# Kernel optimization log

Hardware: AMD Instinct MI355X
Metric: run time of the kernel (lower is better)

## Reference

```python
import jax, jax.numpy as jnp
import numpy as np

B, IN, OUT = 32768, 64, 32
G, P = 8, 3              # bspline grid_size, order
TAY = 4                  # taylor_order
JDEG, JA, JB = 4, 1.0, 1.0
CDEG = 4
FREQ = 8
WCH = 4
TEMP = 2.0               # mix_temperature


def bspline_bases(x):
    # x: (B, In) -> (B, In, G+P)   Cox-de Boor with data-dependent uniform knots
    xmin = x.min(axis=0)
    xmax = x.max(axis=0)
    pad = (xmax - xmin) < 1e-8
    xmin = jnp.where(pad, xmin - 0.5, xmin)
    xmax = jnp.where(pad, xmax + 0.5, xmax)
    t = jnp.linspace(0.0, 1.0, G + 1, dtype=x.dtype)           # (G+1,)
    internal = xmin[:, None] + (xmax - xmin)[:, None] * t[None, :]  # (In, G+1)
    grid = jnp.concatenate([jnp.repeat(internal[:, :1], P, axis=1),
                            internal,
                            jnp.repeat(internal[:, -1:], P, axis=1)], axis=1)  # (In, G+2P+1)
    xe = x[:, :, None]
    bases = ((xe >= grid[:, :-1]) & (xe < grid[:, 1:])).astype(x.dtype)
    mask_last = x == grid[:, -1][None, :]                       # (B, In)
    bases = jnp.where(mask_last[:, :, None], 0.0, bases)
    bases = bases.at[..., -1].set(jnp.where(mask_last, 1.0, bases[..., -1]))
    for r in range(1, P + 1):
        ld = jnp.maximum(grid[:, r:-1] - grid[:, :-(r + 1)], 1e-12)
        rd = jnp.maximum(grid[:, r + 1:] - grid[:, 1:-r], 1e-12)
        left = (xe - grid[:, :-(r + 1)]) / ld * bases[..., :-1]
        right = (grid[:, r + 1:] - xe) / rd * bases[..., 1:]
        bases = left + right
    return bases


def taylor_bases(x):
    k = jnp.arange(TAY, dtype=x.dtype)
    fac = jnp.exp(jax.lax.lgamma(k + 1.0))
    return x[:, :, None] ** k / fac                             # (B, In, TAY)


def jacobi_bases(x):
    a, b = JA, JB
    terms = [jnp.ones_like(x)]
    if JDEG >= 1:
        terms.append(0.5 * (2.0 * (a + 1.0) * x + (a - b)) / np.sqrt(2.0))
    for n in range(2, JDEG + 1):
        k = n - 1
        A1 = 2 * k + a + b
        A2 = 2 * (k + 1) * (k + a + b + 1) * (A1 + 1)
        A3 = (A1 + 1) * ((A1 + 2) * A1 * x + a * a - b * b)
        A4 = 2 * (k + a) * (k + b) * (A1 + 2)
        Jn = A3 / A2 * terms[n - 1] - A4 / A2 * terms[n - 2]
        terms.append(Jn / np.sqrt(n + 1.0))
    return jnp.stack(terms, axis=-1)                            # (B, In, JDEG+1)


def cheby_bases(x):
    # project=True: sanitize + clamp
    xc = jnp.where(jnp.isfinite(x), x, 0.0)
    xc = jnp.clip(xc, -1e6, 1e6)
    terms = [jnp.ones_like(xc), xc]
    for _ in range(1, CDEG):
        terms.append(2.0 * xc * terms[-1] - terms[-2])
    T = jnp.stack(terms, axis=-1)                               # (B, In, CDEG+1)
    n = jnp.arange(CDEG + 1, dtype=x.dtype)
    return T / jnp.sqrt(n + 1.0)                                # norm='deg'


def fourier_bases(x):
    k = jnp.arange(1, FREQ + 1, dtype=x.dtype)
    xk = x[:, :, None] * k
    Phi = jnp.concatenate([jnp.cos(xk), jnp.sin(xk)], axis=-1)  # (B, In, 2*FREQ)
    return Phi / np.sqrt(2.0 * FREQ)


def wavelet_bases(x, scale_logit, shift):
    a = jax.nn.softplus(scale_logit) + 1e-6                     # (In, WCH)
    u = (x[:, :, None] - shift[None]) / a[None]                 # (B, In, WCH)
    return (u ** 2 - 1.0) * jnp.exp(-0.5 * u ** 2)              # mexican_hat, norm='none'


def setup_inputs() -> dict:
    key = jax.random.key(0)
    ks = jax.random.split(key, 12)
    f32 = jnp.float32
    return {
        "x": jax.random.normal(ks[0], (B, IN), f32),
        "base_v": jax.random.normal(ks[1], (OUT, IN), f32) / np.sqrt(IN),
        "base_g": jnp.ones((OUT, 1), f32),
        "base_bias": jnp.zeros((OUT,), f32),
        "bspline_coef": 0.1 * jax.random.normal(ks[2], (OUT, IN, G + P), f32),
        "taylor_coef": 0.1 * jax.random.normal(ks[3], (OUT, IN, TAY), f32),
        "jacobi_coef": 0.1 * jax.random.normal(ks[4], (OUT, IN, JDEG + 1), f32),
        "cheby_coef": 0.1 * jax.random.normal(ks[5], (OUT, IN, CDEG + 1), f32),
        "fourier_coef": 0.1 * jax.random.normal(ks[6], (OUT, IN, 2 * FREQ), f32),
        "wavelet_coef": 0.1 * jax.random.normal(ks[7], (OUT, IN, WCH), f32),
        "wavelet_scale_logit": 0.1 * jax.random.normal(ks[8], (IN, WCH), f32),
        "wavelet_shift": jax.random.normal(ks[9], (IN, WCH), f32),
        "gains": jnp.zeros((6,), f32),
        "alpha_logit": jnp.asarray(2.94, f32),
        "beta_logit": jnp.asarray(0.0, f32),
        "mix_logits": 0.1 * jax.random.normal(ks[10], (OUT, IN, 6), f32),
    }


def reference(x, base_v, base_g, base_bias, bspline_coef, taylor_coef, jacobi_coef,
              cheby_coef, fourier_coef, wavelet_coef, wavelet_scale_logit, wavelet_shift,
              gains, alpha_logit, beta_logit, mix_logits):
    sp = jax.nn.softplus
    # weight-normalized base linear (dim=0 => per-output-row norm)
    vnorm = jnp.sqrt(jnp.sum(base_v ** 2, axis=1, keepdims=True))
    W = base_g * base_v / vnorm                                 # (OUT, IN)
    base_out = x @ W.T + base_bias                              # (B, OUT)
    # static per-(o,i) family mixing weights
    mixw = jax.nn.softmax(mix_logits / TEMP, axis=-1)           # (OUT, IN, 6)
    Phis = [bspline_bases(x), taylor_bases(x), jacobi_bases(x), cheby_bases(x),
            fourier_bases(x), wavelet_bases(x, wavelet_scale_logit, wavelet_shift)]
    coefs = [bspline_coef, taylor_coef, jacobi_coef, cheby_coef, fourier_coef, wavelet_coef]
    y_kan = jnp.zeros((x.shape[0], W.shape[0]), dtype=x.dtype)
    for f in range(6):
        coef_eff = coefs[f] * mixw[..., f:f + 1] * sp(gains[f])
        y_kan = y_kan + jnp.einsum('bik,oik->bo', Phis[f], coef_eff)
    return sp(alpha_logit) * base_out + sp(beta_logit) * y_kan
```

## Files before the change

### kernel.cpp

```cpp
#include <hip/hip_runtime.h>
#include <stdint.h>

#define NB   32768
#define NIN  64
#define NOUT 32
#define OFF_PMIN 0
#define OFF_PMAX 16384
#define OFF_FEAT 32768
#define OFF_EB   35840
#define OFF_CSW  35968

typedef __bf16 bf16x8 __attribute__((ext_vector_type(8)));
typedef float  f32x4  __attribute__((ext_vector_type(4)));

__device__ __forceinline__ float softplus_f(float x) {
  return fmaxf(x, 0.0f) + log1pf(expf(-fabsf(x)));
}

__global__ __launch_bounds__(256) void k_minmax(const float* __restrict__ X,
                                                float* __restrict__ pmin,
                                                float* __restrict__ pmax) {
  const float4* X4 = (const float4*)X;
  int t = threadIdx.x;
  int g = t & 15, r = t >> 4;
  float4 lo = {3.402823466e38f, 3.402823466e38f, 3.402823466e38f, 3.402823466e38f};
  float4 hi = {-3.402823466e38f, -3.402823466e38f, -3.402823466e38f, -3.402823466e38f};
  int base = blockIdx.x * 8192;
  #pragma unroll 8
  for (int k = 0; k < 32; ++k) {
    float4 v = X4[base + k * 256 + t];
    lo.x = fminf(lo.x, v.x); lo.y = fminf(lo.y, v.y);
    lo.z = fminf(lo.z, v.z); lo.w = fminf(lo.w, v.w);
    hi.x = fmaxf(hi.x, v.x); hi.y = fmaxf(hi.y, v.y);
    hi.z = fmaxf(hi.z, v.z); hi.w = fmaxf(hi.w, v.w);
  }
  __shared__ float4 slo[16][16], shi[16][16];
  slo[r][g] = lo; shi[r][g] = hi;
  __syncthreads();
  if (t < 64) {
    int gg = t >> 2, c = t & 3;
    float l = 3.402823466e38f, h = -3.402823466e38f;
    #pragma unroll
    for (int rr = 0; rr < 16; ++rr) {
      const float* pl = (const float*)&slo[rr][gg];
      const float* ph = (const float*)&shi[rr][gg];
      l = fminf(l, pl[c]); h = fmaxf(h, ph[c]);
    }
    pmin[blockIdx.x * 64 + t] = l;
    pmax[blockIdx.x * 64 + t] = h;
  }
}

__global__ __launch_bounds__(256) void k_setup(const float* __restrict__ pmin,
                                               const float* __restrict__ pmax,
                                               const float* __restrict__ wscale,
                                               const float* __restrict__ wshift,
                                               const float* __restrict__ alpha,
                                               const float* __restrict__ bias,
                                               const float* __restrict__ base_v,
                                               const float* __restrict__ base_g,
                                               const float* __restrict__ bsp,
                                               const float* __restrict__ tay,
                                               const float* __restrict__ jac,
                                               const float* __restrict__ che,
                                               const float* __restrict__ fou,
                                               const float* __restrict__ wav,
                                               const float* __restrict__ gains,
                                               const float* __restrict__ beta,
                                               const float* __restrict__ mixl,
                                               float* __restrict__ featp,
                                               float* __restrict__ ebias,
                                               unsigned short* __restrict__ Csw) {
  int t = threadIdx.x;
  if (blockIdx.x < 8) {
    int o = blockIdx.x * 4 + (t >> 6);
    int i = t & 63;
    int p = o * 64 + i;
    float spa = softplus_f(alpha[0]);
    float spb = softplus_f(beta[0]);
    float spg[6];
    #pragma unroll
    for (int f = 0; f < 6; ++f) spg[f] = softplus_f(gains[f]);
    float m[6], mmax = -3.402823466e38f;
    #pragma unroll
    for (int f = 0; f < 6; ++f) { m[f] = mixl[p * 6 + f] * 0.5f; mmax = fmaxf(mmax, m[f]); }
    float es = 0.f;
    #pragma unroll
    for (int f = 0; f < 6; ++f) { m[f] = __expf(m[f] - mmax); es += m[f]; }
    float inv = 1.0f / es;

    float vv = base_v[p];
    float s2 = vv * vv;
    #pragma unroll
    for (int d = 1; d < 64; d <<= 1) s2 += __shfl_xor(s2, d);
    float vn = sqrtf(s2);
    float Wid = spa * base_g[o] * vv / vn;

    float wB = spb * spg[0] * m[0] * inv;
    float wT = spb * spg[1] * m[1] * inv;
    float wJ = spb * spg[2] * m[2] * inv;
    float wC = spb * spg[3] * m[3] * inv;
    float wF = spb * spg[4] * m[4] * inv * 0.25f;
    float wW = spb * spg[5] * m[5] * inv;

    float j0 = jac[p * 5 + 0], j1 = jac[p * 5 + 1], j2 = jac[p * 5 + 2],
          j3 = jac[p * 5 + 3], j4 = jac[p * 5 + 4];
    float c0 = che[p * 5 + 0], c1 = che[p * 5 + 1], c2 = che[p * 5 + 2],
          c3 = che[p * 5 + 3], c4 = che[p * 5 + 4];
    float t0 = tay[p * 4 + 0], t1 = tay[p * 4 + 1], t2 = tay[p * 4 + 2], t3 = tay[p * 4 + 3];

    float slot[40];
    #pragma unroll
    for (int k = 0; k < 11; ++k) slot[k] = wB * bsp[p * 11 + k];
    slot[11] = Wid + wT * t1
             + wJ * (1.4142136f * j1 - 0.7619780f * j3)
             + wC * (0.7071068f * c1 - 1.5f * c3);
    slot[12] = wT * 0.5f * t2
             + wJ * (1.2247449f * j2 - 0.9736894f * j4)
             + wC * (1.1547005f * c2 - 3.5777088f * c4);
    slot[13] = wT * (1.0f / 6.0f) * t3
             + wJ * 0.9797959f * j3
             + wC * 2.0f * c3;
    slot[14] = wJ * 0.7302967f * j4 + wC * 3.5777088f * c4;
    slot[15] = wT * t0
             + wJ * (j0 - 0.3464102f * j2 + 0.1147551f * j4)
             + wC * (c0 - 0.5773503f * c2 + 0.4472136f * c4);
    #pragma unroll
    for (int k = 0; k < 8; ++k) slot[16 + k] = wF * fou[p * 16 + k];
    #pragma unroll
    for (int k = 0; k < 8; ++k) slot[24 + k] = wF * fou[p * 16 + 8 + k];
    #pragma unroll
    for (int k = 0; k < 4; ++k) slot[32 + k] = wW * wav[p * 4 + k];
    slot[36] = 0.f; slot[37] = 0.f; slot[38] = 0.f; slot[39] = 0.f;

    int wv = i >> 4, kgi = (i >> 2) & 3, cc = i & 3;
    bf16x8* CBo = reinterpret_cast<bf16x8*>(Csw);
    #pragma unroll
    for (int s = 0; s < 5; ++s) {
      bf16x8 pk;
      #pragma unroll
      for (int j = 0; j < 8; ++j) pk[j] = (__bf16)slot[s * 8 + j];
      int st = wv * 20 + cc * 5 + s;
      CBo[(st * 4 + kgi) * 32 + o] = pk;
    }
  } else {
    __shared__ float slo[4][64], shi[4][64];
    int i = t & 63, cg = t >> 6;
    float lo = 3.402823466e38f, hi = -3.402823466e38f;
    #pragma unroll
    for (int pp = 0; pp < 16; ++pp) {
      int p = pp * 4 + cg;
      lo = fminf(lo, pmin[p * 64 + i]);
      hi = fmaxf(hi, pmax[p * 64 + i]);
    }
    slo[cg][i] = lo; shi[cg][i] = hi;
    __syncthreads();
    if (t < 64) {
      lo = fminf(fminf(slo[0][t], slo[1][t]), fminf(slo[2][t], slo[3][t]));
      hi = fmaxf(fmaxf(shi[0][t], shi[1][t]), fmaxf(shi[2][t], shi[3][t]));
      if (hi - lo < 1e-8f) { lo = lo - 0.5f; hi = hi + 0.5f; }
      float d = hi - lo;
      float* fp = featp + t * 12;
      fp[0] = lo;
      fp[1] = 8.0f / d;
      #pragma unroll
      for (int c = 0; c < 4; ++c) {
        float a = softplus_f(wscale[t * 4 + c]) + 1e-6f;
        fp[2 + c] = 1.0f / a;
        fp[6 + c] = wshift[t * 4 + c];
      }
      fp[10] = 0.f; fp[11] = 0.f;
    }
    if (t >= 128 && t < 160) {
      int o = t - 128;
      ebias[o] = softplus_f(alpha[0]) * bias[o];
    }
  }
}

__device__ __forceinline__ void basis40(float x, float4 q0, float4 q1, float4 q2,
                                        bf16x8& A0, bf16x8& A1, bf16x8& A2,
                                        bf16x8& A3, bf16x8& A4) {
  {
    float u = (x - q0.x) * q0.y;
    int ji = (int)u;
    float e0 = (ji == 0) ? 1.f : 0.f;
    float e1 = (ji == 1) ? 1.f : 0.f;
    float e2 = (ji == 2) ? 1.f : 0.f;
    float e3 = (ji == 3) ? 1.f : 0.f;
    float e4 = (ji == 4) ? 1.f : 0.f;
    float e5 = (ji == 5) ? 1.f : 0.f;
    float e6 = (ji == 6) ? 1.f : 0.f;
    float e7 = (ji == 7) ? 1.f : 0.f;
    float d0 = u,       d1 = u - 1.f, d2 = u - 2.f, d3 = u - 3.f, d4 = u - 4.f;
    float d5 = u - 5.f, d6 = u - 6.f, d7 = u - 7.f, d8 = u - 8.f;
    float a2 = -d1 * e0;
    float a3 = d0 * e0 - d2 * e1;
    float a4 = d1 * e1 - d3 * e2;
    float a5 = d2 * e2 - d4 * e3;
    float a6 = d3 * e3 - d5 * e4;
    float a7 = d4 * e4 - d6 * e5;
    float a8 = d5 * e5 - d7 * e6;
    float a9 = d6 * e6 - d8 * e7;
    float a10 = d7 * e7;
    float h0 = 0.5f * d0, h1 = 0.5f * d1, h2 = 0.5f * d2, h3 = 0.5f * d3, h4 = 0.5f * d4;
    float h5 = 0.5f * d5, h6 = 0.5f * d6, h7 = 0.5f * d7, h8 = 0.5f * d8;
    float c1v = -d1 * a2;
    float c2v = d0 * a2 - h2 * a3;
    float c3v = h0 * a3 - h3 * a4;
    float c4v = h1 * a4 - h4 * a5;
    float c5v = h2 * a5 - h5 * a6;
    float c6v = h3 * a6 - h6 * a7;
    float c7v = h4 * a7 - h7 * a8;
    float c8v = h5 * a8 - h8 * a9;
    float c9v = h6 * a9 - d8 * a10;
    float c10v = d7 * a10;
    const float TH = 0.33333333333333f;
    A0[0] = (__bf16)(-d1 * c1v);
    A0[1] = (__bf16)(d0 * c1v - h2 * c2v);
    A0[2] = (__bf16)(h0 * c2v - TH * (d3 * c3v));
    A0[3] = (__bf16)((d0 * c3v - d4 * c4v) * TH);
    A0[4] = (__bf16)((d1 * c4v - d5 * c5v) * TH);
    A0[5] = (__bf16)((d2 * c5v - d6 * c6v) * TH);
    A0[6] = (__bf16)((d3 * c6v - d7 * c7v) * TH);
    A0[7] = (__bf16)((d4 * c7v - d8 * c8v) * TH);
    A1[0] = (__bf16)(TH * (d5 * c8v) - h8 * c9v);
    A1[1] = (__bf16)(h6 * c9v - d8 * c10v);
    A1[2] = (__bf16)(d7 * c10v);
  }
  {
    float x2 = x * x, x3v = x2 * x, x4v = x2 * x2;
    A1[3] = (__bf16)x;
    A1[4] = (__bf16)x2;
    A1[5] = (__bf16)x3v;
    A1[6] = (__bf16)x4v;
    A1[7] = (__bf16)1.0f;
  }
  {
    float s1 = __sinf(x), c1f = __cosf(x);
    float c2f = 2.0f * c1f * c1f - 1.0f, s2f = 2.0f * s1 * c1f;
    float c3f = c2f * c1f - s2f * s1,    s3f = s2f * c1f + c2f * s1;
    float c4f = 2.0f * c2f * c2f - 1.0f, s4f = 2.0f * s2f * c2f;
    float c5f = c4f * c1f - s4f * s1,    s5f = s4f * c1f + c4f * s1;
    float c6f = c4f * c2f - s4f * s2f,   s6f = s4f * c2f + c4f * s2f;
    float c7f = c4f * c3f - s4f * s3f,   s7f = s4f * c3f + c4f * s3f;
    float c8f = 2.0f * c4f * c4f - 1.0f, s8f = 2.0f * s4f * c4f;
    A2[0] = (__bf16)c1f; A2[1] = (__bf16)c2f; A2[2] = (__bf16)c3f; A2[3] = (__bf16)c4f;
    A2[4] = (__bf16)c5f; A2[5] = (__bf16)c6f; A2[6] = (__bf16)c7f; A2[7] = (__bf16)c8f;
    A3[0] = (__bf16)s1;  A3[1] = (__bf16)s2f; A3[2] = (__bf16)s3f; A3[3] = (__bf16)s4f;
    A3[4] = (__bf16)s5f; A3[5] = (__bf16)s6f; A3[6] = (__bf16)s7f; A3[7] = (__bf16)s8f;
  }
  {
    float u0 = (x - q1.z) * q0.z, u1 = (x - q1.w) * q0.w;
    float u2 = (x - q2.x) * q1.x, u3 = (x - q2.y) * q1.y;
    float s0 = u0 * u0, s1w = u1 * u1, s2w = u2 * u2, s3 = u3 * u3;
    A4[0] = (__bf16)((s0 - 1.0f) * __expf(-0.5f * s0));
    A4[1] = (__bf16)((s1w - 1.0f) * __expf(-0.5f * s1w));
    A4[2] = (__bf16)((s2w - 1.0f) * __expf(-0.5f * s2w));
    A4[3] = (__bf16)((s3 - 1.0f) * __expf(-0.5f * s3));
    A4[4] = (__bf16)0.0f; A4[5] = (__bf16)0.0f;
    A4[6] = (__bf16)0.0f; A4[7] = (__bf16)0.0f;
  }
}

__global__ __launch_bounds__(256) void k_main(const float* __restrict__ X,
                                              const unsigned short* __restrict__ Csw,
                                              const float* __restrict__ featp,
                                              const float* __restrict__ ebias,
                                              float* __restrict__ out) {
  __shared__ float red[3][1024];

  int t = threadIdx.x;
  int w = t >> 6, lane = t & 63;
  int col = lane & 15, kg = lane >> 4;
  int sbase = blockIdx.x * 32;

  const float4* X4 = (const float4*)X;
  float4 xq0 = X4[(sbase + col) * 16 + w * 4 + kg];
  float4 xq1 = X4[(sbase + 16 + col) * 16 + w * 4 + kg];
  float xr0[4] = {xq0.x, xq0.y, xq0.z, xq0.w};
  float xr1[4] = {xq1.x, xq1.y, xq1.z, xq1.w};

  f32x4 acc00 = {0.f, 0.f, 0.f, 0.f};
  f32x4 acc01 = {0.f, 0.f, 0.f, 0.f};
  f32x4 acc10 = {0.f, 0.f, 0.f, 0.f};
  f32x4 acc11 = {0.f, 0.f, 0.f, 0.f};
  const bf16x8* CB = reinterpret_cast<const bf16x8*>(Csw);
  const bf16x8* CBw = CB + (size_t)w * 2560 + kg * 32;

  bf16x8 B0, B1, B2, B3, B4, B5, B6, B7, B8, B9;
#define LOADB(cc) do { const bf16x8* p_ = CBw + (size_t)(cc) * 640;            \
    B0 = p_[col];        B1 = p_[col + 16];                                    \
    B2 = p_[128 + col];  B3 = p_[128 + col + 16];                              \
    B4 = p_[256 + col];  B5 = p_[256 + col + 16];                              \
    B6 = p_[384 + col];  B7 = p_[384 + col + 16];                              \
    B8 = p_[512 + col];  B9 = p_[512 + col + 16]; } while (0)

  LOADB(0);

  #pragma unroll 1
  for (int c = 0; c < 4; ++c) {
    int f = w * 16 + kg * 4 + c;
    const float4* fq = (const float4*)(featp + f * 12);
    float4 q0 = fq[0];
    float4 q1 = fq[1];
    float4 q2 = fq[2];

    bf16x8 A0, A1, A2, A3, A4;

    basis40(xr0[c], q0, q1, q2, A0, A1, A2, A3, A4);
    acc00 = __builtin_amdgcn_mfma_f32_16x16x32_bf16(A0, B0, acc00, 0, 0, 0);
    acc01 = __builtin_amdgcn_mfma_f32_16x16x32_bf16(A0, B1, acc01, 0, 0, 0);
    acc00 = __builtin_amdgcn_mfma_f32_16x16x32_bf16(A1, B2, acc00, 0, 0, 0);
    acc01 = __builtin_amdgcn_mfma_f32_16x16x32_bf16(A1, B3, acc01, 0, 0, 0);
    acc00 = __builtin_amdgcn_mfma_f32_16x16x32_bf16(A2, B4, acc00, 0, 0, 0);
    acc01 = __builtin_amdgcn_mfma_f32_16x16x32_bf16(A2, B5, acc01, 0, 0, 0);
    acc00 = __builtin_amdgcn_mfma_f32_16x16x32_bf16(A3, B6, acc00, 0, 0, 0);
    acc01 = __builtin_amdgcn_mfma_f32_16x16x32_bf16(A3, B7, acc01, 0, 0, 0);
    acc00 = __builtin_amdgcn_mfma_f32_16x16x32_bf16(A4, B8, acc00, 0, 0, 0);
    acc01 = __builtin_amdgcn_mfma_f32_16x16x32_bf16(A4, B9, acc01, 0, 0, 0);

    basis40(xr1[c], q0, q1, q2, A0, A1, A2, A3, A4);
    acc10 = __builtin_amdgcn_mfma_f32_16x16x32_bf16(A0, B0, acc10, 0, 0, 0);
    acc11 = __builtin_amdgcn_mfma_f32_16x16x32_bf16(A0, B1, acc11, 0, 0, 0);
    acc10 = __builtin_amdgcn_mfma_f32_16x16x32_bf16(A1, B2, acc10, 0, 0, 0);
    acc11 = __builtin_amdgcn_mfma_f32_16x16x32_bf16(A1, B3, acc11, 0, 0, 0);
    acc10 = __builtin_amdgcn_mfma_f32_16x16x32_bf16(A2, B4, acc10, 0, 0, 0);
    acc11 = __builtin_amdgcn_mfma_f32_16x16x32_bf16(A2, B5, acc11, 0, 0, 0);
    acc10 = __builtin_amdgcn_mfma_f32_16x16x32_bf16(A3, B6, acc10, 0, 0, 0);
    acc11 = __builtin_amdgcn_mfma_f32_16x16x32_bf16(A3, B7, acc11, 0, 0, 0);
    acc10 = __builtin_amdgcn_mfma_f32_16x16x32_bf16(A4, B8, acc10, 0, 0, 0);
    acc11 = __builtin_amdgcn_mfma_f32_16x16x32_bf16(A4, B9, acc11, 0, 0, 0);

    if (c < 3) LOADB(c + 1);
  }
#undef LOADB

  if (w > 0) {
    float* rw = &red[w - 1][0];
    #pragma unroll
    for (int j = 0; j < 4; ++j) {
      int idx = (kg * 4 + j) * 32 + col;
      rw[idx]            = acc00[j];
      rw[idx + 16]       = acc01[j];
      rw[512 + idx]      = acc10[j];
      rw[512 + idx + 16] = acc11[j];
    }
  }
  __syncthreads();
  if (w == 0) {
    float eb0 = ebias[col], eb1 = ebias[col + 16];
    #pragma unroll
    for (int j = 0; j < 4; ++j) {
      int idx0 = (kg * 4 + j) * 32 + col;
      int idx1 = idx0 + 16;
      int row0 = sbase + kg * 4 + j;
      int row1 = row0 + 16;
      out[row0 * 32 + col]      = acc00[j] + red[0][idx0] + red[1][idx0] + red[2][idx0] + eb0;
      out[row0 * 32 + col + 16] = acc01[j] + red[0][idx1] + red[1][idx1] + red[2][idx1] + eb1;
      out[row1 * 32 + col]      = acc10[j] + red[0][512 + idx0] + red[1][512 + idx0] + red[2][512 + idx0] + eb0;
      out[row1 * 32 + col + 16] = acc11[j] + red[0][512 + idx1] + red[1][512 + idx1] + red[2][512 + idx1] + eb1;
    }
  }
}

extern "C" void kernel_launch(void* const* d_in, const int* in_sizes, int n_in,
                              void* d_out, int out_size, void* d_ws, size_t ws_size,
                              hipStream_t stream) {
  const float* X   = (const float*)d_in[0];
  const float* bv  = (const float*)d_in[1];
  const float* bg  = (const float*)d_in[2];
  const float* bbi = (const float*)d_in[3];
  const float* bsp = (const float*)d_in[4];
  const float* tay = (const float*)d_in[5];
  const float* jac = (const float*)d_in[6];
  const float* che = (const float*)d_in[7];
  const float* fou = (const float*)d_in[8];
  const float* wav = (const float*)d_in[9];
  const float* wsc = (const float*)d_in[10];
  const float* wsh = (const float*)d_in[11];
  const float* gns = (const float*)d_in[12];
  const float* alp = (const float*)d_in[13];
  const float* bet = (const float*)d_in[14];
  const float* mxl = (const float*)d_in[15];
  float* out = (float*)d_out;

  uint8_t* w = (uint8_t*)d_ws;
  float* pmin  = (float*)(w + OFF_PMIN);
  float* pmax  = (float*)(w + OFF_PMAX);
  float* featp = (float*)(w + OFF_FEAT);
  float* ebias = (float*)(w + OFF_EB);
  unsigned short* Csw = (unsigned short*)(w + OFF_CSW);

  k_minmax<<<64, 256, 0, stream>>>(X, pmin, pmax);
  k_setup<<<9, 256, 0, stream>>>(pmin, pmax, wsc, wsh, alp, bbi,
                                 bv, bg, bsp, tay, jac, che, fou, wav,
                                 gns, bet, mxl, featp, ebias, Csw);
  k_main<<<1024, 256, 0, stream>>>(X, Csw, featp, ebias, out);
}
```

Baseline: 32.57 us.

## Merge minmax and coefficient setup into one kernel, finalize features in main

Fuses the min/max reduction and the coefficient packing into a single prep kernel, so the pipeline uses two launches instead of three. The final min/max reduction, the per-feature parameters and the bias are now recomputed redundantly in every main-kernel block and kept in shared memory. This removes a launch and a serial dependency stage. In exchange, each of the 1024 blocks does an extra 16 KB read, a reduction and two barriers before its MFMA loop. Launch bounds on the main kernel now also request 3 blocks per CU.

After: 30.29 us. 1.08x faster.

```diff
diff --git a/kernel.cpp b/kernel.cpp
--- a/kernel.cpp
+++ b/kernel.cpp
@@ -6,9 +6,7 @@
 #define NOUT 32
 #define OFF_PMIN 0
 #define OFF_PMAX 16384
-#define OFF_FEAT 32768
-#define OFF_EB   35840
-#define OFF_CSW  35968
+#define OFF_CSW  32768
 
 typedef __bf16 bf16x8 __attribute__((ext_vector_type(8)));
 typedef float  f32x4  __attribute__((ext_vector_type(4)));
@@ -17,63 +15,54 @@
   return fmaxf(x, 0.0f) + log1pf(expf(-fabsf(x)));
 }
 
-__global__ __launch_bounds__(256) void k_minmax(const float* __restrict__ X,
-                                                float* __restrict__ pmin,
-                                                float* __restrict__ pmax) {
-  const float4* X4 = (const float4*)X;
+__global__ __launch_bounds__(256) void k_prep(const float* __restrict__ X,
+                                              const float* __restrict__ base_v,
+                                              const float* __restrict__ base_g,
+                                              const float* __restrict__ bsp,
+                                              const float* __restrict__ tay,
+                                              const float* __restrict__ jac,
+                                              const float* __restrict__ che,
+                                              const float* __restrict__ fou,
+                                              const float* __restrict__ wav,
+                                              const float* __restrict__ gains,
+                                              const float* __restrict__ alpha,
+                                              const float* __restrict__ beta,
+                                              const float* __restrict__ mixl,
+                                              float* __restrict__ pmin,
+                                              float* __restrict__ pmax,
+                                              unsigned short* __restrict__ Csw) {
   int t = threadIdx.x;
-  int g = t & 15, r = t >> 4;
-  float4 lo = {3.402823466e38f, 3.402823466e38f, 3.402823466e38f, 3.402823466e38f};
-  float4 hi = {-3.402823466e38f, -3.402823466e38f, -3.402823466e38f, -3.402823466e38f};
-  int base = blockIdx.x * 8192;
-  #pragma unroll 8
-  for (int k = 0; k < 32; ++k) {
-    float4 v = X4[base + k * 256 + t];
-    lo.x = fminf(lo.x, v.x); lo.y = fminf(lo.y, v.y);
-    lo.z = fminf(lo.z, v.z); lo.w = fminf(lo.w, v.w);
-    hi.x = fmaxf(hi.x, v.x); hi.y = fmaxf(hi.y, v.y);
-    hi.z = fmaxf(hi.z, v.z); hi.w = fmaxf(hi.w, v.w);
-  }
-  __shared__ float4 slo[16][16], shi[16][16];
-  slo[r][g] = lo; shi[r][g] = hi;
-  __syncthreads();
-  if (t < 64) {
-    int gg = t >> 2, c = t & 3;
-    float l = 3.402823466e38f, h = -3.402823466e38f;
-    #pragma unroll
-    for (int rr = 0; rr < 16; ++rr) {
-      const float* pl = (const float*)&slo[rr][gg];
-      const float* ph = (const float*)&shi[rr][gg];
-      l = fminf(l, pl[c]); h = fmaxf(h, ph[c]);
-    }
-    pmin[blockIdx.x * 64 + t] = l;
-    pmax[blockIdx.x * 64 + t] = h;
-  }
-}
-
-__global__ __launch_bounds__(256) void k_setup(const float* __restrict__ pmin,
-                                               const float* __restrict__ pmax,
-                                               const float* __restrict__ wscale,
-                                               const float* __restrict__ wshift,
-                                               const float* __restrict__ alpha,
-                                               const float* __restrict__ bias,
-                                               const float* __restrict__ base_v,
-                                               const float* __restrict__ base_g,
-                                               const float* __restrict__ bsp,
-                                               const float* __restrict__ tay,
-                                               const float* __restrict__ jac,
-                                               const float* __restrict__ che,
-                                               const float* __restrict__ fou,
-                                               const float* __restrict__ wav,
-                                               const float* __restrict__ gains,
-                                               const float* __restrict__ beta,
-                                               const float* __restrict__ mixl,
-                                               float* __restrict__ featp,
-                                               float* __restrict__ ebias,
-                                               unsigned short* __restrict__ Csw) {
-  int t = threadIdx.x;
-  if (blockIdx.x < 8) {
-    int o = blockIdx.x * 4 + (t >> 6);
+  if (blockIdx.x < 64) {
+    const float4* X4 = (const float4*)X;
+    int g = t & 15, r = t >> 4;
+    float4 lo = {3.402823466e38f, 3.402823466e38f, 3.402823466e38f, 3.402823466e38f};
+    float4 hi = {-3.402823466e38f, -3.402823466e38f, -3.402823466e38f, -3.402823466e38f};
+    int base = blockIdx.x * 8192;
+    #pragma unroll 8
+    for (int k = 0; k < 32; ++k) {
+      float4 v = X4[base + k * 256 + t];
+      lo.x = fminf(lo.x, v.x); lo.y = fminf(lo.y, v.y);
+      lo.z = fminf(lo.z, v.z); lo.w = fminf(lo.w, v.w);
+      hi.x = fmaxf(hi.x, v.x); hi.y = fmaxf(hi.y, v.y);
+      hi.z = fmaxf(hi.z, v.z); hi.w = fmaxf(hi.w, v.w);
+    }
+    __shared__ float4 slo[16][16], shi[16][16];
+    slo[r][g] = lo; shi[r][g] = hi;
+    __syncthreads();
+    if (t < 64) {
+      int gg = t >> 2, c = t & 3;
+      float l = 3.402823466e38f, h = -3.402823466e38f;
+      #pragma unroll
+      for (int rr = 0; rr < 16; ++rr) {
+        const float* pl = (const float*)&slo[rr][gg];
+        const float* ph = (const float*)&shi[rr][gg];
+        l = fminf(l, pl[c]); h = fmaxf(h, ph[c]);
+      }
+      pmin[blockIdx.x * 64 + t] = l;
+      pmax[blockIdx.x * 64 + t] = h;
+    }
+  } else {
+    int o = (blockIdx.x - 64) * 4 + (t >> 6);
     int i = t & 63;
     int p = o * 64 + i;
     float spa = softplus_f(alpha[0]);
@@ -103,8 +92,8 @@
     float wF = spb * spg[4] * m[4] * inv * 0.25f;
     float wW = spb * spg[5] * m[5] * inv;
 
-    float j0 = jac[p * 5 + 0], j1 = jac[p * 5 + 1], j2 = jac[p * 5 + 2],
-          j3 = jac[p * 5 + 3], j4 = jac[p * 5 + 4];
+    float j1 = jac[p * 5 + 1], j2 = jac[p * 5 + 2], j3 = jac[p * 5 + 3], j4 = jac[p * 5 + 4];
+    float j0 = jac[p * 5 + 0];
     float c0 = che[p * 5 + 0], c1 = che[p * 5 + 1], c2 = che[p * 5 + 2],
           c3 = che[p * 5 + 3], c4 = che[p * 5 + 4];
     float t0 = tay[p * 4 + 0], t1 = tay[p * 4 + 1], t2 = tay[p * 4 + 2], t3 = tay[p * 4 + 3];
@@ -142,38 +131,6 @@
       for (int j = 0; j < 8; ++j) pk[j] = (__bf16)slot[s * 8 + j];
       int st = wv * 20 + cc * 5 + s;
       CBo[(st * 4 + kgi) * 32 + o] = pk;
-    }
-  } else {
-    __shared__ float slo[4][64], shi[4][64];
-    int i = t & 63, cg = t >> 6;
-    float lo = 3.402823466e38f, hi = -3.402823466e38f;
-    #pragma unroll
-    for (int pp = 0; pp < 16; ++pp) {
-      int p = pp * 4 + cg;
-      lo = fminf(lo, pmin[p * 64 + i]);
-      hi = fmaxf(hi, pmax[p * 64 + i]);
-    }
-    slo[cg][i] = lo; shi[cg][i] = hi;
-    __syncthreads();
-    if (t < 64) {
-      lo = fminf(fminf(slo[0][t], slo[1][t]), fminf(slo[2][t], slo[3][t]));
-      hi = fmaxf(fmaxf(shi[0][t], shi[1][t]), fmaxf(shi[2][t], shi[3][t]));
-      if (hi - lo < 1e-8f) { lo = lo - 0.5f; hi = hi + 0.5f; }
-      float d = hi - lo;
-      float* fp = featp + t * 12;
-      fp[0] = lo;
-      fp[1] = 8.0f / d;
-      #pragma unroll
-      for (int c = 0; c < 4; ++c) {
-        float a = softplus_f(wscale[t * 4 + c]) + 1e-6f;
-        fp[2 + c] = 1.0f / a;
-        fp[6 + c] = wshift[t * 4 + c];
-      }
-      fp[10] = 0.f; fp[11] = 0.f;
-    }
-    if (t >= 128 && t < 160) {
-      int o = t - 128;
-      ebias[o] = softplus_f(alpha[0]) * bias[o];
     }
   }
 }
@@ -263,12 +220,19 @@
   }
 }
 
-__global__ __launch_bounds__(256) void k_main(const float* __restrict__ X,
-                                              const unsigned short* __restrict__ Csw,
-                                              const float* __restrict__ featp,
-                                              const float* __restrict__ ebias,
-                                              float* __restrict__ out) {
+__global__ __launch_bounds__(256, 3) void k_main(const float* __restrict__ X,
+                                                 const unsigned short* __restrict__ Csw,
+                                                 const float* __restrict__ pmin,
+                                                 const float* __restrict__ pmax,
+                                                 const float* __restrict__ wscale,
+                                                 const float* __restrict__ wshift,
+                                                 const float* __restrict__ alpha,
+                                                 const float* __restrict__ bias,
+                                                 float* __restrict__ out) {
   __shared__ float red[3][1024];
+  __shared__ float slo[4][64], shi[4][64];
+  __shared__ float featL[64][12];
+  __shared__ float ebL[32];
 
   int t = threadIdx.x;
   int w = t >> 6, lane = t & 63;
@@ -281,13 +245,8 @@
   float xr0[4] = {xq0.x, xq0.y, xq0.z, xq0.w};
   float xr1[4] = {xq1.x, xq1.y, xq1.z, xq1.w};
 
-  f32x4 acc00 = {0.f, 0.f, 0.f, 0.f};
-  f32x4 acc01 = {0.f, 0.f, 0.f, 0.f};
-  f32x4 acc10 = {0.f, 0.f, 0.f, 0.f};
-  f32x4 acc11 = {0.f, 0.f, 0.f, 0.f};
   const bf16x8* CB = reinterpret_cast<const bf16x8*>(Csw);
   const bf16x8* CBw = CB + (size_t)w * 2560 + kg * 32;
-
   bf16x8 B0, B1, B2, B3, B4, B5, B6, B7, B8, B9;
 #define LOADB(cc) do { const bf16x8* p_ = CBw + (size_t)(cc) * 640;            \
     B0 = p_[col];        B1 = p_[col + 16];                                    \
@@ -295,13 +254,50 @@
     B4 = p_[256 + col];  B5 = p_[256 + col + 16];                              \
     B6 = p_[384 + col];  B7 = p_[384 + col + 16];                              \
     B8 = p_[512 + col];  B9 = p_[512 + col + 16]; } while (0)
-
   LOADB(0);
+
+  {
+    int f = t & 63, q = t >> 6;
+    float lo = 3.402823466e38f, hi = -3.402823466e38f;
+    #pragma unroll
+    for (int pp = 0; pp < 16; ++pp) {
+      int p = q * 16 + pp;
+      lo = fminf(lo, pmin[p * 64 + f]);
+      hi = fmaxf(hi, pmax[p * 64 + f]);
+    }
+    slo[q][f] = lo; shi[q][f] = hi;
+  }
+  __syncthreads();
+  if (t < 64) {
+    float lo = fminf(fminf(slo[0][t], slo[1][t]), fminf(slo[2][t], slo[3][t]));
+    float hi = fmaxf(fmaxf(shi[0][t], shi[1][t]), fmaxf(shi[2][t], shi[3][t]));
+    if (hi - lo < 1e-8f) { lo = lo - 0.5f; hi = hi + 0.5f; }
+    float d = hi - lo;
+    featL[t][0] = lo;
+    featL[t][1] = 8.0f / d;
+    #pragma unroll
+    for (int c = 0; c < 4; ++c) {
+      float a = softplus_f(wscale[t * 4 + c]) + 1e-6f;
+      featL[t][2 + c] = 1.0f / a;
+      featL[t][6 + c] = wshift[t * 4 + c];
+    }
+    featL[t][10] = 0.f; featL[t][11] = 0.f;
+  }
+  if (t >= 128 && t < 160) {
+    int o = t - 128;
+    ebL[o] = softplus_f(alpha[0]) * bias[o];
+  }
+  __syncthreads();
+
+  f32x4 acc00 = {0.f, 0.f, 0.f, 0.f};
+  f32x4 acc01 = {0.f, 0.f, 0.f, 0.f};
+  f32x4 acc10 = {0.f, 0.f, 0.f, 0.f};
+  f32x4 acc11 = {0.f, 0.f, 0.f, 0.f};
 
   #pragma unroll 1
   for (int c = 0; c < 4; ++c) {
     int f = w * 16 + kg * 4 + c;
-    const float4* fq = (const float4*)(featp + f * 12);
+    const float4* fq = (const float4*)&featL[f][0];
     float4 q0 = fq[0];
     float4 q1 = fq[1];
     float4 q2 = fq[2];
@@ -349,7 +345,7 @@
   }
   __syncthreads();
   if (w == 0) {
-    float eb0 = ebias[col], eb1 = ebias[col + 16];
+    float eb0 = ebL[col], eb1 = ebL[col + 16];
     #pragma unroll
     for (int j = 0; j < 4; ++j) {
       int idx0 = (kg * 4 + j) * 32 + col;
@@ -386,15 +382,11 @@
   float* out = (float*)d_out;
 
   uint8_t* w = (uint8_t*)d_ws;
-  float* pmin  = (float*)(w + OFF_PMIN);
-  float* pmax  = (float*)(w + OFF_PMAX);
-  float* featp = (float*)(w + OFF_FEAT);
-  float* ebias = (float*)(w + OFF_EB);
+  float* pmin = (float*)(w + OFF_PMIN);
+  float* pmax = (float*)(w + OFF_PMAX);
   unsigned short* Csw = (unsigned short*)(w + OFF_CSW);
 
-  k_minmax<<<64, 256, 0, stream>>>(X, pmin, pmax);
-  k_setup<<<9, 256, 0, stream>>>(pmin, pmax, wsc, wsh, alp, bbi,
-                                 bv, bg, bsp, tay, jac, che, fou, wav,
-                                 gns, bet, mxl, featp, ebias, Csw);
-  k_main<<<1024, 256, 0, stream>>>(X, Csw, featp, ebias, out);
-}
+  k_prep<<<72, 256, 0, stream>>>(X, bv, bg, bsp, tay, jac, che, fou, wav,
+                                 gns, alp, bet, mxl, pmin, pmax, Csw);
+  k_main<<<1024, 256, 0, stream>>>(X, Csw, pmin, pmax, wsc, wsh, alp, bbi, out);
+}
```
